# Kernel tuning notes

Measured on AMD Instinct MI355X. Metric: run time of the kernel, lower is better.

## Reference

```python
import jax, jax.numpy as jnp
import numpy as np

T = 16384
G = 8
D_IN = 2048
D_OUT = 8192
# uneven per-expert group sizes summing exactly to T (torch.split requires this)
_GROUP_SIZES = np.array([1024, 3072, 2048, 512, 4096, 1536, 2560, 1536], dtype=np.int64)
assert _GROUP_SIZES.sum() == T


def setup_inputs() -> dict:
    key = jax.random.key(0)
    k_x, k_w = jax.random.split(key)
    hidden_states = jax.random.normal(k_x, (T, D_IN), dtype=jnp.float32)
    # kaiming_uniform_(a=sqrt(5)) on [G, out, in] -> bound = 1/sqrt(in_features)
    bound = 1.0 / np.sqrt(D_IN)
    weight = jax.random.uniform(k_w, (G, D_OUT, D_IN), dtype=jnp.float32,
                                minval=-bound, maxval=bound)
    offsets = jnp.asarray(np.cumsum(_GROUP_SIZES), dtype=jnp.int64)
    return {"hidden_states": hidden_states, "offsets": offsets, "weight": weight}


def reference(hidden_states, offsets, weight):
    # grouped GEMM: for group g, rows [offsets[g-1]:offsets[g]] @ weight[g].T
    # weight is [G, out, in]; torch transposes last two dims -> rhs [G, in, out]
    group_sizes = jnp.diff(offsets, prepend=jnp.zeros((1,), offsets.dtype)).astype(jnp.int32)
    rhs = jnp.swapaxes(weight, -1, -2)  # [G, in, out]
    return jax.lax.ragged_dot(hidden_states, rhs, group_sizes)  # [T, out]
```

## Files before the change

kernel.cpp:

```cpp
#include <hip/hip_runtime.h>
#include <stdint.h>

#define T_TOK   16384
#define D_INK   2048
#define D_OUTN  8192
#define G_NUM   8

#define BM 256
#define BN 256
#define BK 64
#define NKT (D_INK / BK)
#define MT_TILES (T_TOK / BM)
#define NT_TILES (D_OUTN / BN)
#define MCHUNK 4

typedef __attribute__((ext_vector_type(8))) short bf16x8;
typedef __attribute__((ext_vector_type(4))) float f32x4;

#define BARRIER() do { asm volatile("" ::: "memory"); __builtin_amdgcn_s_barrier(); asm volatile("" ::: "memory"); } while (0)
#define LGKM0()   asm volatile("s_waitcnt lgkmcnt(0)" ::: "memory")
#define VMCNT(n)  asm volatile("s_waitcnt vmcnt(" #n ")" ::: "memory")

__device__ __forceinline__ unsigned int f2bf(float f) {
    union { float f; unsigned int u; } v; v.f = f;
    unsigned int u = v.u;
    unsigned int r = u + 0x7FFFu + ((u >> 16) & 1u);
    return r >> 16;
}

__global__ __launch_bounds__(256) void cvt_f32_bf16(const float* __restrict__ src,
                                                    unsigned short* __restrict__ dst,
                                                    long long n8) {
    long long i = (long long)blockIdx.x * blockDim.x + threadIdx.x;
    long long stride = (long long)gridDim.x * blockDim.x;
    const float4* s4 = reinterpret_cast<const float4*>(src);
    for (; i < n8; i += stride) {
        float4 x = s4[i * 2];
        float4 y = s4[i * 2 + 1];
        uint4 o;
        o.x = f2bf(x.x) | (f2bf(x.y) << 16);
        o.y = f2bf(x.z) | (f2bf(x.w) << 16);
        o.z = f2bf(y.x) | (f2bf(y.y) << 16);
        o.w = f2bf(y.z) | (f2bf(y.w) << 16);
        *reinterpret_cast<uint4*>(dst + i * 8) = o;
    }
}

__device__ __forceinline__ void gload_lds16(const unsigned short* g, void* l) {
    __builtin_amdgcn_global_load_lds(
        (const __attribute__((address_space(1))) void*)g,
        (__attribute__((address_space(3))) void*)l,
        16, 0, 0);
}

__global__ __launch_bounds__(512, 2) void grouped_gemm_256(
    const unsigned short* __restrict__ Abf,
    const unsigned short* __restrict__ Wbf,
    const int* __restrict__ offs_raw,
    float* __restrict__ out)
{
    __shared__ unsigned short lds[2][32768];

    const int tid  = threadIdx.x;
    const int wave = tid >> 6;
    const int lane = tid & 63;

    const int swz = (blockIdx.x & 7) * (MT_TILES * NT_TILES / 8) + (blockIdx.x >> 3);
    const int per_chunk = MCHUNK * NT_TILES;
    const int chunk = swz / per_chunk;
    const int rem   = swz % per_chunk;
    const int nt = rem >> 2;
    const int mt = chunk * MCHUNK + (rem & (MCHUNK - 1));

    const int row0 = mt * BM;
    const int col0 = nt * BN;

    const int ostride = (offs_raw[1] == 0) ? 2 : 1;
    int g = 0;
#pragma unroll
    for (int i = 0; i < G_NUM - 1; ++i)
        if (row0 >= offs_raw[i * ostride]) g = i + 1;

    const unsigned short* Aorig = Abf + (size_t)row0 * D_INK;
    const unsigned short* Worig = Wbf + ((size_t)g * D_OUTN + col0) * D_INK;

    const int lrow = lane >> 2;
    const int gcol_off = ((lane & 3) * 8) ^ ((lane & 32) ? 16 : 0);

    const int fr  = lane & 15;
    const int fk2 = (lane >> 4) << 4;
    const int swz_off = fr * 64 + (fk2 ^ ((fr & 8) ? 32 : 0));
    const int wm16 = (wave >> 2) * 8;
    const int wn16 = (wave & 3) * 4;
    const int wm = (wave >> 2) * 128;
    const int wn = (wave & 3) * 64;

    char* ldsc = (char*)&lds[0][0];

    auto stageA = [&](int buf, int kt) {
#pragma unroll
        for (int i = 0; i < 4; ++i) {
            const int s = wave * 4 + i;
            const int sr = s >> 1, sc = s & 1;
            const unsigned short* src = Aorig + (size_t)(sr * 16 + lrow) * D_INK
                                        + kt * BK + sc * 32 + gcol_off;
            gload_lds16(src, ldsc + buf * 65536 + s * 1024);
        }
    };
    auto stageB = [&](int buf, int kt) {
#pragma unroll
        for (int i = 0; i < 4; ++i) {
            const int s = wave * 4 + i;
            const int sr = s >> 1, sc = s & 1;
            const unsigned short* src = Worig + (size_t)(sr * 16 + lrow) * D_INK
                                        + kt * BK + sc * 32 + gcol_off;
            gload_lds16(src, ldsc + buf * 65536 + 32768 + s * 1024);
        }
    };
    auto ldA = [&](int buf, int sr, int ks) -> bf16x8 {
        return *reinterpret_cast<const bf16x8*>(ldsc + buf * 65536 + (sr * 2 + ks) * 1024 + swz_off);
    };
    auto ldB = [&](int buf, int sr, int ks) -> bf16x8 {
        return *reinterpret_cast<const bf16x8*>(ldsc + buf * 65536 + 32768 + (sr * 2 + ks) * 1024 + swz_off);
    };

    f32x4 acc[8][4] = {};
    bf16x8 a[4][2], b[4][2];

    stageB(0, 0); stageA(0, 0);
    stageB(1, 1); stageA(1, 1);
    VMCNT(8);
    BARRIER();

    for (int t = 0; t < NKT; ++t) {
        const int buf = t & 1;

#pragma unroll
        for (int i = 0; i < 4; ++i) { a[i][0] = ldA(buf, wm16 + i, 0); a[i][1] = ldA(buf, wm16 + i, 1); }
#pragma unroll
        for (int j = 0; j < 2; ++j) { b[j][0] = ldB(buf, wn16 + j, 0); b[j][1] = ldB(buf, wn16 + j, 1); }
        BARRIER();
        LGKM0();
        __builtin_amdgcn_s_setprio(1);
#pragma unroll
        for (int i = 0; i < 4; ++i)
#pragma unroll
            for (int j = 0; j < 2; ++j) {
                acc[i][j] = __builtin_amdgcn_mfma_f32_16x16x32_bf16(a[i][0], b[j][0], acc[i][j], 0, 0, 0);
                acc[i][j] = __builtin_amdgcn_mfma_f32_16x16x32_bf16(a[i][1], b[j][1], acc[i][j], 0, 0, 0);
            }
        __builtin_amdgcn_s_setprio(0);
        BARRIER();

#pragma unroll
        for (int j = 2; j < 4; ++j) { b[j][0] = ldB(buf, wn16 + j, 0); b[j][1] = ldB(buf, wn16 + j, 1); }
        BARRIER();
        LGKM0();
        __builtin_amdgcn_s_setprio(1);
#pragma unroll
        for (int i = 0; i < 4; ++i)
#pragma unroll
            for (int j = 2; j < 4; ++j) {
                acc[i][j] = __builtin_amdgcn_mfma_f32_16x16x32_bf16(a[i][0], b[j][0], acc[i][j], 0, 0, 0);
                acc[i][j] = __builtin_amdgcn_mfma_f32_16x16x32_bf16(a[i][1], b[j][1], acc[i][j], 0, 0, 0);
            }
        __builtin_amdgcn_s_setprio(0);
        BARRIER();

#pragma unroll
        for (int i = 0; i < 4; ++i) { a[i][0] = ldA(buf, wm16 + 4 + i, 0); a[i][1] = ldA(buf, wm16 + 4 + i, 1); }
        if (t + 2 < NKT) stageB(buf, t + 2);
        BARRIER();
        LGKM0();
        __builtin_amdgcn_s_setprio(1);
#pragma unroll
        for (int i = 0; i < 4; ++i)
#pragma unroll
            for (int j = 0; j < 2; ++j) {
                acc[4 + i][j] = __builtin_amdgcn_mfma_f32_16x16x32_bf16(a[i][0], b[j][0], acc[4 + i][j], 0, 0, 0);
                acc[4 + i][j] = __builtin_amdgcn_mfma_f32_16x16x32_bf16(a[i][1], b[j][1], acc[4 + i][j], 0, 0, 0);
            }
        __builtin_amdgcn_s_setprio(0);
        BARRIER();

        if (t + 2 < NKT) stageA(buf, t + 2);
        BARRIER();
        __builtin_amdgcn_s_setprio(1);
#pragma unroll
        for (int i = 0; i < 4; ++i)
#pragma unroll
            for (int j = 2; j < 4; ++j) {
                acc[4 + i][j] = __builtin_amdgcn_mfma_f32_16x16x32_bf16(a[i][0], b[j][0], acc[4 + i][j], 0, 0, 0);
                acc[4 + i][j] = __builtin_amdgcn_mfma_f32_16x16x32_bf16(a[i][1], b[j][1], acc[4 + i][j], 0, 0, 0);
            }
        __builtin_amdgcn_s_setprio(0);
        if (t + 2 < NKT)      { VMCNT(8); }
        else if (t + 1 < NKT) { VMCNT(0); }
        BARRIER();
    }

    const int crb = (lane >> 4) * 4;
#pragma unroll
    for (int i = 0; i < 8; ++i)
#pragma unroll
        for (int j = 0; j < 4; ++j)
#pragma unroll
            for (int r = 0; r < 4; ++r) {
                const int rr = row0 + wm + i * 16 + crb + r;
                const int cc = col0 + wn + j * 16 + fr;
                out[(size_t)rr * D_OUTN + cc] = acc[i][j][r];
            }
}

__global__ __launch_bounds__(256) void naive_grouped(
    const float* __restrict__ A, const float* __restrict__ W,
    const int* __restrict__ offs_raw, float* __restrict__ out)
{
    const long long total = (long long)T_TOK * D_OUTN;
    long long idx = (long long)blockIdx.x * blockDim.x + threadIdx.x;
    const long long stride = (long long)gridDim.x * blockDim.x;
    const int ostride = (offs_raw[1] == 0) ? 2 : 1;
    for (; idx < total; idx += stride) {
        const int t = (int)(idx / D_OUTN);
        const int c = (int)(idx % D_OUTN);
        int g = 0;
        for (int i = 0; i < G_NUM - 1; ++i)
            if (t >= offs_raw[i * ostride]) g = i + 1;
        const float4* a4 = reinterpret_cast<const float4*>(A + (size_t)t * D_INK);
        const float4* w4 = reinterpret_cast<const float4*>(W + ((size_t)g * D_OUTN + c) * D_INK);
        float s = 0.f;
        for (int k = 0; k < D_INK / 4; ++k) {
            float4 av = a4[k], wv = w4[k];
            s += av.x * wv.x + av.y * wv.y + av.z * wv.z + av.w * wv.w;
        }
        out[idx] = s;
    }
}

extern "C" void kernel_launch(void* const* d_in, const int* in_sizes, int n_in,
                              void* d_out, int out_size, void* d_ws, size_t ws_size,
                              hipStream_t stream) {
    const float* hidden = (const float*)d_in[0];
    const int*   offs   = (const int*)d_in[1];
    const float* weight = (const float*)d_in[2];
    float* out = (float*)d_out;

    const size_t nA = (size_t)T_TOK * D_INK;
    const size_t nW = (size_t)G_NUM * D_OUTN * D_INK;
    const size_t need = (nA + nW) * sizeof(unsigned short);

    if (ws_size >= need) {
        unsigned short* Abf = (unsigned short*)d_ws;
        unsigned short* Wbf = Abf + nA;
        cvt_f32_bf16<<<2048, 256, 0, stream>>>(hidden, Abf, (long long)(nA / 8));
        cvt_f32_bf16<<<4096, 256, 0, stream>>>(weight, Wbf, (long long)(nW / 8));
        grouped_gemm_256<<<MT_TILES * NT_TILES, 512, 0, stream>>>(Abf, Wbf, offs, out);
    } else {
        naive_grouped<<<8192, 256, 0, stream>>>(hidden, weight, offs, out);
    }
}
```

Before: 794.1 us.

## Restagger global-to-LDS prefetch into half-tile chunks across MFMA phases

```diff
diff --git a/kernel.cpp b/kernel.cpp
--- a/kernel.cpp
+++ b/kernel.cpp
@@ -20,6 +20,7 @@
 #define BARRIER() do { asm volatile("" ::: "memory"); __builtin_amdgcn_s_barrier(); asm volatile("" ::: "memory"); } while (0)
 #define LGKM0()   asm volatile("s_waitcnt lgkmcnt(0)" ::: "memory")
 #define VMCNT(n)  asm volatile("s_waitcnt vmcnt(" #n ")" ::: "memory")
+#define MFMA16(d,va,vb) d = __builtin_amdgcn_mfma_f32_16x16x32_bf16(va, vb, d, 0, 0, 0)
 
 __device__ __forceinline__ unsigned int f2bf(float f) {
     union { float f; unsigned int u; } v; v.f = f;
@@ -97,105 +98,101 @@
 
     char* ldsc = (char*)&lds[0][0];
 
-    auto stageA = [&](int buf, int kt) {
-#pragma unroll
-        for (int i = 0; i < 4; ++i) {
-            const int s = wave * 4 + i;
+    auto stageAh = [&](int buf, int kt, int h) {
+#pragma unroll
+        for (int i = 0; i < 2; ++i) {
+            const int s = h * 16 + i * 8 + wave;
             const int sr = s >> 1, sc = s & 1;
             const unsigned short* src = Aorig + (size_t)(sr * 16 + lrow) * D_INK
                                         + kt * BK + sc * 32 + gcol_off;
             gload_lds16(src, ldsc + buf * 65536 + s * 1024);
         }
     };
-    auto stageB = [&](int buf, int kt) {
-#pragma unroll
-        for (int i = 0; i < 4; ++i) {
-            const int s = wave * 4 + i;
+    auto stageBh = [&](int buf, int kt, int h) {
+#pragma unroll
+        for (int i = 0; i < 2; ++i) {
+            const int s = h * 16 + i * 8 + wave;
             const int sr = s >> 1, sc = s & 1;
             const unsigned short* src = Worig + (size_t)(sr * 16 + lrow) * D_INK
                                         + kt * BK + sc * 32 + gcol_off;
             gload_lds16(src, ldsc + buf * 65536 + 32768 + s * 1024);
         }
     };
-    auto ldA = [&](int buf, int sr, int ks) -> bf16x8 {
-        return *reinterpret_cast<const bf16x8*>(ldsc + buf * 65536 + (sr * 2 + ks) * 1024 + swz_off);
-    };
-    auto ldB = [&](int buf, int sr, int ks) -> bf16x8 {
-        return *reinterpret_cast<const bf16x8*>(ldsc + buf * 65536 + 32768 + (sr * 2 + ks) * 1024 + swz_off);
-    };
 
     f32x4 acc[8][4] = {};
     bf16x8 a[4][2], b[4][2];
 
-    stageB(0, 0); stageA(0, 0);
-    stageB(1, 1); stageA(1, 1);
-    VMCNT(8);
-    BARRIER();
-
-    for (int t = 0; t < NKT; ++t) {
-        const int buf = t & 1;
-
-#pragma unroll
-        for (int i = 0; i < 4; ++i) { a[i][0] = ldA(buf, wm16 + i, 0); a[i][1] = ldA(buf, wm16 + i, 1); }
-#pragma unroll
-        for (int j = 0; j < 2; ++j) { b[j][0] = ldB(buf, wn16 + j, 0); b[j][1] = ldB(buf, wn16 + j, 1); }
-        BARRIER();
-        LGKM0();
+    auto ldA4 = [&](int buf, int mb) {
+#pragma unroll
+        for (int i = 0; i < 4; ++i) {
+            const int sr = wm16 + mb + i;
+            a[i][0] = *reinterpret_cast<const bf16x8*>(ldsc + buf * 65536 + (sr * 2 + 0) * 1024 + swz_off);
+            a[i][1] = *reinterpret_cast<const bf16x8*>(ldsc + buf * 65536 + (sr * 2 + 1) * 1024 + swz_off);
+        }
+    };
+    auto ldB2 = [&](int buf, int jb) {
+#pragma unroll
+        for (int j = 0; j < 2; ++j) {
+            const int sr = wn16 + jb + j;
+            b[jb + j][0] = *reinterpret_cast<const bf16x8*>(ldsc + buf * 65536 + 32768 + (sr * 2 + 0) * 1024 + swz_off);
+            b[jb + j][1] = *reinterpret_cast<const bf16x8*>(ldsc + buf * 65536 + 32768 + (sr * 2 + 1) * 1024 + swz_off);
+        }
+    };
+    auto quad = [&](int ib, int jb) {
         __builtin_amdgcn_s_setprio(1);
 #pragma unroll
         for (int i = 0; i < 4; ++i)
 #pragma unroll
             for (int j = 0; j < 2; ++j) {
-                acc[i][j] = __builtin_amdgcn_mfma_f32_16x16x32_bf16(a[i][0], b[j][0], acc[i][j], 0, 0, 0);
-                acc[i][j] = __builtin_amdgcn_mfma_f32_16x16x32_bf16(a[i][1], b[j][1], acc[i][j], 0, 0, 0);
+                MFMA16(acc[ib + i][jb + j], a[i][0], b[jb + j][0]);
+                MFMA16(acc[ib + i][jb + j], a[i][1], b[jb + j][1]);
             }
         __builtin_amdgcn_s_setprio(0);
-        BARRIER();
-
-#pragma unroll
-        for (int j = 2; j < 4; ++j) { b[j][0] = ldB(buf, wn16 + j, 0); b[j][1] = ldB(buf, wn16 + j, 1); }
-        BARRIER();
-        LGKM0();
-        __builtin_amdgcn_s_setprio(1);
-#pragma unroll
-        for (int i = 0; i < 4; ++i)
-#pragma unroll
-            for (int j = 2; j < 4; ++j) {
-                acc[i][j] = __builtin_amdgcn_mfma_f32_16x16x32_bf16(a[i][0], b[j][0], acc[i][j], 0, 0, 0);
-                acc[i][j] = __builtin_amdgcn_mfma_f32_16x16x32_bf16(a[i][1], b[j][1], acc[i][j], 0, 0, 0);
-            }
-        __builtin_amdgcn_s_setprio(0);
-        BARRIER();
-
-#pragma unroll
-        for (int i = 0; i < 4; ++i) { a[i][0] = ldA(buf, wm16 + 4 + i, 0); a[i][1] = ldA(buf, wm16 + 4 + i, 1); }
-        if (t + 2 < NKT) stageB(buf, t + 2);
-        BARRIER();
-        LGKM0();
-        __builtin_amdgcn_s_setprio(1);
-#pragma unroll
-        for (int i = 0; i < 4; ++i)
-#pragma unroll
-            for (int j = 0; j < 2; ++j) {
-                acc[4 + i][j] = __builtin_amdgcn_mfma_f32_16x16x32_bf16(a[i][0], b[j][0], acc[4 + i][j], 0, 0, 0);
-                acc[4 + i][j] = __builtin_amdgcn_mfma_f32_16x16x32_bf16(a[i][1], b[j][1], acc[4 + i][j], 0, 0, 0);
-            }
-        __builtin_amdgcn_s_setprio(0);
-        BARRIER();
-
-        if (t + 2 < NKT) stageA(buf, t + 2);
-        BARRIER();
-        __builtin_amdgcn_s_setprio(1);
-#pragma unroll
-        for (int i = 0; i < 4; ++i)
-#pragma unroll
-            for (int j = 2; j < 4; ++j) {
-                acc[4 + i][j] = __builtin_amdgcn_mfma_f32_16x16x32_bf16(a[i][0], b[j][0], acc[4 + i][j], 0, 0, 0);
-                acc[4 + i][j] = __builtin_amdgcn_mfma_f32_16x16x32_bf16(a[i][1], b[j][1], acc[4 + i][j], 0, 0, 0);
-            }
-        __builtin_amdgcn_s_setprio(0);
-        if (t + 2 < NKT)      { VMCNT(8); }
-        else if (t + 1 < NKT) { VMCNT(0); }
+    };
+
+    stageBh(0, 0, 0); stageBh(0, 0, 1);
+    stageAh(0, 0, 0); stageAh(0, 0, 1);
+    stageBh(1, 1, 0); stageBh(1, 1, 1);
+    VMCNT(4);
+    BARRIER();
+
+    for (int t = 0; t < NKT; t += 2) {
+        const bool s2 = (t + 2 < NKT), s3 = (t + 3 < NKT);
+
+        ldA4(0, 0); ldB2(0, 0);
+        stageAh(1, t + 1, 0);
+        BARRIER(); LGKM0(); quad(0, 0); BARRIER();
+
+        ldB2(0, 2);
+        stageAh(1, t + 1, 1);
+        BARRIER(); LGKM0(); quad(0, 2); BARRIER();
+
+        ldA4(0, 4);
+        if (s2) stageBh(0, t + 2, 0);
+        BARRIER(); LGKM0(); quad(4, 0); BARRIER();
+
+        if (s2) stageBh(0, t + 2, 1);
+        BARRIER();
+        quad(4, 2);
+        if (s2) { VMCNT(4); } else { VMCNT(0); }
+        BARRIER();
+
+        ldA4(1, 0); ldB2(1, 0);
+        if (s2) stageAh(0, t + 2, 0);
+        BARRIER(); LGKM0(); quad(0, 0); BARRIER();
+
+        ldB2(1, 2);
+        if (s2) stageAh(0, t + 2, 1);
+        BARRIER(); LGKM0(); quad(0, 2); BARRIER();
+
+        ldA4(1, 4);
+        if (s3) stageBh(1, t + 3, 0);
+        BARRIER(); LGKM0(); quad(4, 0); BARRIER();
+
+        if (s3) stageBh(1, t + 3, 1);
+        BARRIER();
+        quad(4, 2);
+        if (s3) { VMCNT(4); } else { VMCNT(0); }
         BARRIER();
     }
 
```

Result: faster. 710.7 us (-10.5%).
